# Performance work log

Hardware: AMD Instinct MI355X
Metric: run time of the kernel (lower is better)

Reference implementation:

```python
import jax, jax.numpy as jnp
import numpy as np

S, B, C = 7, 2, 20
LAMBDA_COORD = 5.0
LAMBDA_NOOBJ = 0.5
EPS = 1e-6


def setup_inputs() -> dict:
    key = jax.random.key(0)
    k1, k2 = jax.random.split(key)
    N = 16384
    predictions = jax.random.normal(k1, (N, S, S, B * 5 + C), dtype=jnp.float32)
    targets = jax.random.normal(k2, (N, S, S, B * 5 + C), dtype=jnp.float32)
    return {"predictions": predictions, "targets": targets}


def _iou(b1, b2):
    # b1: [..., B, 4], b2: [..., 1, 4]; boxes are (x, y, w, h)
    b1x1 = b1[..., 0] - b1[..., 2] / 2
    b1y1 = b1[..., 1] - b1[..., 3] / 2
    b1x2 = b1[..., 0] + b1[..., 2] / 2
    b1y2 = b1[..., 1] + b1[..., 3] / 2
    b2x1 = b2[..., 0] - b2[..., 2] / 2
    b2y1 = b2[..., 1] - b2[..., 3] / 2
    b2x2 = b2[..., 0] + b2[..., 2] / 2
    b2y2 = b2[..., 1] + b2[..., 3] / 2
    inter = jnp.clip(jnp.minimum(b1x2, b2x2) - jnp.maximum(b1x1, b2x1), 0, None) * \
            jnp.clip(jnp.minimum(b1y2, b2y2) - jnp.maximum(b1y1, b2y1), 0, None)
    union = b1[..., 2] * b1[..., 3] + b2[..., 2] * b2[..., 3] - inter
    return inter / (union + EPS)


def reference(predictions, targets):
    N = predictions.shape[0]
    pred_boxes = predictions[..., : B * 5].reshape(N, S, S, B, 5)  # [N,S,S,B,5]
    tgt_box = targets[..., :5]                                     # [N,S,S,5]

    ious = _iou(pred_boxes[..., :4], tgt_box[..., None, :4])       # [N,S,S,B]
    # Replicate loop semantics: best starts at (iou=0, idx=0), strict '>' update
    best_idx = jnp.argmax(jnp.where(ious > 0, ious, 0.0), axis=-1)  # [N,S,S]
    best_box = jnp.take_along_axis(
        pred_boxes, best_idx[..., None, None], axis=3
    )[..., 0, :]                                                    # [N,S,S,5]

    obj = (tgt_box[..., 4] > 0).astype(predictions.dtype)          # [N,S,S]

    # Localization loss
    xy_err = jnp.sum((best_box[..., :2] - tgt_box[..., :2]) ** 2, axis=-1)
    wh_err = jnp.sum(
        (jnp.sqrt(jnp.clip(best_box[..., 2:4], EPS, None)) -
         jnp.sqrt(jnp.clip(tgt_box[..., 2:4], EPS, None))) ** 2, axis=-1)
    coord_loss = jnp.sum(obj * (xy_err + wh_err)) / N

    # Confidence losses
    conf_obj_loss = jnp.sum(obj * (best_box[..., 4] - tgt_box[..., 4]) ** 2) / N
    conf_sq = pred_boxes[..., 4] ** 2                              # [N,S,S,B]
    conf_sq_all = jnp.sum(conf_sq, axis=-1)
    conf_sq_best = jnp.take_along_axis(conf_sq, best_idx[..., None], axis=-1)[..., 0]
    conf_noobj_loss = jnp.sum(obj * (conf_sq_all - conf_sq_best) +
                              (1.0 - obj) * conf_sq_all) / N

    # Classification loss (only for object cells)
    cls_err = jnp.sum((predictions[..., B * 5:] - targets[..., B * 5:]) ** 2, axis=-1)
    class_loss = jnp.sum(obj * cls_err) / N

    total = (LAMBDA_COORD * coord_loss + conf_obj_loss +
             LAMBDA_NOOBJ * conf_noobj_loss + class_loss)
    return total
```

## Files before the change

kernel.cpp:

```cpp
#include <hip/hip_runtime.h>


constexpr float LC   = 5.0f;
constexpr float LN   = 0.5f;
constexpr float EPSF = 1e-6f;

__device__ __forceinline__ float iou_pair(
    float cx1, float cy1, float w1, float h1,
    float cx2, float cy2, float w2, float h2) {
  float b1x1 = cx1 - w1 * 0.5f, b1x2 = cx1 + w1 * 0.5f;
  float b1y1 = cy1 - h1 * 0.5f, b1y2 = cy1 + h1 * 0.5f;
  float b2x1 = cx2 - w2 * 0.5f, b2x2 = cx2 + w2 * 0.5f;
  float b2y1 = cy2 - h2 * 0.5f, b2y2 = cy2 + h2 * 0.5f;
  float iw = fmaxf(fminf(b1x2, b2x2) - fmaxf(b1x1, b2x1), 0.0f);
  float ih = fmaxf(fminf(b1y2, b2y2) - fmaxf(b1y1, b2y1), 0.0f);
  float inter = iw * ih;
  float uni = w1 * h1 + w2 * h2 - inter;
  return inter / (uni + EPSF);
}

__global__ __launch_bounds__(256) void yolo_cell_kernel(
    const float* __restrict__ pred, const float* __restrict__ tgt,
    float* __restrict__ partial, int ncells, float invN) {
  int cell = blockIdx.x * 256 + threadIdx.x;
  float contrib = 0.0f;
  if (cell < ncells) {
    const float* p = pred + (size_t)cell * 30;
    const float* t = tgt  + (size_t)cell * 30;
    float2 p01 = *(const float2*)(p + 0);
    float2 p23 = *(const float2*)(p + 2);
    float2 p45 = *(const float2*)(p + 4);
    float2 p67 = *(const float2*)(p + 6);
    float2 p89 = *(const float2*)(p + 8);
    float2 t01 = *(const float2*)(t + 0);
    float2 t23 = *(const float2*)(t + 2);
    float2 t45 = *(const float2*)(t + 4);

    float iou0 = iou_pair(p01.x, p01.y, p23.x, p23.y, t01.x, t01.y, t23.x, t23.y);
    float iou1 = iou_pair(p45.y, p67.x, p67.y, p89.x, t01.x, t01.y, t23.x, t23.y);
    float v0 = iou0 > 0.0f ? iou0 : 0.0f;
    float v1 = iou1 > 0.0f ? iou1 : 0.0f;
    bool pick1 = v1 > v0;

    float bx = pick1 ? p45.y : p01.x;
    float by = pick1 ? p67.x : p01.y;
    float bw = pick1 ? p67.y : p23.x;
    float bh = pick1 ? p89.x : p23.y;
    float bc = pick1 ? p89.y : p45.x;

    float obj = t45.x > 0.0f ? 1.0f : 0.0f;

    float dx = bx - t01.x, dy = by - t01.y;
    float xy = dx * dx + dy * dy;
    float sw = sqrtf(fmaxf(bw, EPSF)) - sqrtf(fmaxf(t23.x, EPSF));
    float sh = sqrtf(fmaxf(bh, EPSF)) - sqrtf(fmaxf(t23.y, EPSF));
    float wh = sw * sw + sh * sh;

    float dc = bc - t45.x;

    float sq0 = p45.x * p45.x, sq1 = p89.y * p89.y;
    float sq_all  = sq0 + sq1;
    float sq_best = pick1 ? sq1 : sq0;
    float noobj = obj * (sq_all - sq_best) + (1.0f - obj) * sq_all;

    float cls = 0.0f;
#pragma unroll
    for (int j = 10; j < 30; j += 2) {
      float2 pc = *(const float2*)(p + j);
      float2 tc = *(const float2*)(t + j);
      float d0 = pc.x - tc.x, d1 = pc.y - tc.y;
      cls += d0 * d0 + d1 * d1;
    }

    contrib = (LC * obj * (xy + wh) + obj * dc * dc + LN * noobj + obj * cls) * invN;
  }

  for (int off = 32; off > 0; off >>= 1)
    contrib += __shfl_down(contrib, off);
  __shared__ float wsum[4];
  int lane = threadIdx.x & 63;
  int wid  = threadIdx.x >> 6;
  if (lane == 0) wsum[wid] = contrib;
  __syncthreads();
  if (threadIdx.x == 0)
    partial[blockIdx.x] = (wsum[0] + wsum[1]) + (wsum[2] + wsum[3]);
}

__global__ __launch_bounds__(256) void yolo_final_kernel(
    const float* __restrict__ partial, int n, float* __restrict__ out) {
  double s = 0.0;
  for (int i = threadIdx.x; i < n; i += 256) s += (double)partial[i];
  for (int off = 32; off > 0; off >>= 1) s += __shfl_down(s, off);
  __shared__ double wsum[4];
  int lane = threadIdx.x & 63;
  int wid  = threadIdx.x >> 6;
  if (lane == 0) wsum[wid] = s;
  __syncthreads();
  if (threadIdx.x == 0)
    out[0] = (float)((wsum[0] + wsum[1]) + (wsum[2] + wsum[3]));
}

extern "C" void kernel_launch(void* const* d_in, const int* in_sizes, int n_in,
                              void* d_out, int out_size, void* d_ws, size_t ws_size,
                              hipStream_t stream) {
  const float* pred = (const float*)d_in[0];
  const float* tgt  = (const float*)d_in[1];
  float* out = (float*)d_out;
  float* partial = (float*)d_ws;

  int ncells  = in_sizes[0] / 30;
  int nblocks = (ncells + 255) / 256;
  int N       = ncells / 49;
  float invN  = 1.0f / (float)N;

  yolo_cell_kernel<<<nblocks, 256, 0, stream>>>(pred, tgt, partial, ncells, invN);
  yolo_final_kernel<<<1, 256, 0, stream>>>(partial, nblocks, out);
}
```

Baseline: 37.68 us.

## Stage cell data through LDS with coalesced float4 loads

Each block now copies its 256 cells of predictions and targets into shared memory with fully coalesced float4 loads, then every thread reads its own 30-float cell from LDS. Before this, each thread issued strided float2 global loads spaced 120 bytes apart, which coalesce poorly. The cost is 60 KB of LDS per block, which limits occupancy to about one block per CU and adds a barrier. The per-thread LDS reads at a stride of 30 floats may also cause bank conflicts.

```diff
diff --git a/kernel.cpp b/kernel.cpp
--- a/kernel.cpp
+++ b/kernel.cpp
@@ -19,14 +19,37 @@
   return inter / (uni + EPSF);
 }
 
-__global__ __launch_bounds__(256) void yolo_cell_kernel(
+__global__ __launch_bounds__(256) void yolo_cell_lds(
     const float* __restrict__ pred, const float* __restrict__ tgt,
     float* __restrict__ partial, int ncells, float invN) {
-  int cell = blockIdx.x * 256 + threadIdx.x;
+  __shared__ float sp[256 * 30];
+  __shared__ float st[256 * 30];
+
+  const int tid = threadIdx.x;
+  const long base4  = (long)blockIdx.x * 1920;
+  const long nf4tot = (long)ncells * 30 / 4;
+
+  const float4* p4 = (const float4*)pred;
+  const float4* t4 = (const float4*)tgt;
+  float4* sp4 = (float4*)sp;
+  float4* st4 = (float4*)st;
+
+#pragma unroll
+  for (int j = 0; j < 8; ++j) {
+    int idx = j * 256 + tid;
+    if (idx < 1920 && base4 + idx < nf4tot) {
+      sp4[idx] = p4[base4 + idx];
+      st4[idx] = t4[base4 + idx];
+    }
+  }
+  __syncthreads();
+
+  int cell = blockIdx.x * 256 + tid;
   float contrib = 0.0f;
   if (cell < ncells) {
-    const float* p = pred + (size_t)cell * 30;
-    const float* t = tgt  + (size_t)cell * 30;
+    const float* p = sp + tid * 30;
+    const float* t = st + tid * 30;
+
     float2 p01 = *(const float2*)(p + 0);
     float2 p23 = *(const float2*)(p + 2);
     float2 p45 = *(const float2*)(p + 4);
@@ -78,11 +101,11 @@
   for (int off = 32; off > 0; off >>= 1)
     contrib += __shfl_down(contrib, off);
   __shared__ float wsum[4];
-  int lane = threadIdx.x & 63;
-  int wid  = threadIdx.x >> 6;
+  int lane = tid & 63;
+  int wid  = tid >> 6;
   if (lane == 0) wsum[wid] = contrib;
   __syncthreads();
-  if (threadIdx.x == 0)
+  if (tid == 0)
     partial[blockIdx.x] = (wsum[0] + wsum[1]) + (wsum[2] + wsum[3]);
 }
 
@@ -113,6 +136,6 @@
   int N       = ncells / 49;
   float invN  = 1.0f / (float)N;
 
-  yolo_cell_kernel<<<nblocks, 256, 0, stream>>>(pred, tgt, partial, ncells, invN);
+  yolo_cell_lds<<<nblocks, 256, 0, stream>>>(pred, tgt, partial, ncells, invN);
   yolo_final_kernel<<<1, 256, 0, stream>>>(partial, nblocks, out);
 }
```

Measured after the change: 44.37 us. 17.7% more time.
